# Kernel tuning notes

Measured on AMD Instinct MI355X. Metric: run time of the kernel, lower is better.

The kernel has to match this reference:

```python
import jax, jax.numpy as jnp
import numpy as np

B, C, MX, MY, MZ = 4, 64, 48, 48, 48
A, E = 64, 128  # n_atoms, mol_embed_size
V = MX * MY * MZ


def setup_inputs() -> dict:
    key = jax.random.key(0)
    ks = jax.random.split(key, 12)
    inp = {
        "x": jax.random.normal(ks[0], (B, C, MX, MY, MZ), dtype=jnp.float32),
        "mol_embed": jax.random.normal(ks[1], (B, A, E), dtype=jnp.float32),
        "pos": jax.random.uniform(ks[2], (B, A, 3), dtype=jnp.float32),
        "origin": jnp.zeros((B, 3), dtype=jnp.float32),
        "lattice": jax.random.uniform(ks[3], (B, 3, 3), dtype=jnp.float32) + 0.5,
        "batch_nodes": jax.random.randint(ks[4], (B,), 32, A + 1, dtype=jnp.int32),
        "v_w": jax.random.normal(ks[5], (C, E), dtype=jnp.float32) / np.sqrt(E),
        "v_b": jax.random.normal(ks[6], (C,), dtype=jnp.float32) * 0.01,
        "out_w": jax.random.normal(ks[7], (C, 2 * C), dtype=jnp.float32) / np.sqrt(2 * C),
        "out_b": jax.random.normal(ks[8], (C,), dtype=jnp.float32) * 0.01,
        "conv_w": jax.random.normal(ks[9], (C, C, 3, 3, 3), dtype=jnp.float32) / np.sqrt(C * 27),
        "conv_b": jax.random.normal(ks[10], (C,), dtype=jnp.float32) * 0.01,
    }
    return inp


def _grid_points(o, ldiag):
    # torch.linspace(o, o+l, n) inclusive endpoints -> t = arange(n)/(n-1)
    axes = [o[i] + ldiag[i] * (jnp.arange(n, dtype=jnp.float32) / (n - 1))
            for i, n in enumerate((MX, MY, MZ))]
    gx, gy, gz = jnp.meshgrid(*axes, indexing="ij")
    return jnp.stack([gx, gy, gz], axis=-1).reshape(-1, 3)  # [V,3]


def _forward(x, mol_embed, pos, origin, lattice, batch_nodes,
             v_w, v_b, out_w, out_b, conv_w, conv_b):
    b = x.shape[0]
    ldiag = jnp.diagonal(lattice, axis1=-2, axis2=-1)           # [b,3]
    grid = jax.vmap(_grid_points)(origin, ldiag)                # [b,V,3]
    # pairwise distances via |g|^2 + |p|^2 - 2 g.p (avoids [b,V,A,3])
    g2 = jnp.sum(grid * grid, axis=-1)                          # [b,V]
    p2 = jnp.sum(pos * pos, axis=-1)                            # [b,A]
    gp = jnp.einsum("bvd,bad->bva", grid, pos)                  # [b,V,A]
    d2 = g2[:, :, None] + p2[:, None, :] - 2.0 * gp
    dist = jnp.sqrt(jnp.maximum(d2, 1e-12))
    # ragged mask: atoms >= batch_nodes[i] get -inf score
    valid = jnp.arange(A)[None, None, :] < batch_nodes[:, None, None]
    weight = jnp.where(valid, -dist, -jnp.inf)
    att = jax.nn.softmax(weight, axis=-1)                       # [b,V,A]
    v = mol_embed @ v_w.T + v_b                                 # [b,A,C]
    v = jnp.einsum("bva,bac->bvc", att, v)                      # [b,V,C]
    xv = x.reshape(b, C, V).transpose(0, 2, 1)                  # [b,V,C]
    h = jnp.concatenate([xv, v], axis=-1)                       # [b,V,2C]
    h = jax.nn.relu(h @ out_w.T + out_b)                        # [b,V,C]
    h = h.transpose(0, 2, 1).reshape(b, C, MX, MY, MZ)
    hp = jnp.pad(h, ((0, 0), (0, 0), (1, 1), (1, 1), (1, 1)), mode="wrap")
    conv = jax.lax.conv_general_dilated(
        hp, conv_w, window_strides=(1, 1, 1), padding="VALID",
        dimension_numbers=("NCDHW", "OIDHW", "NCDHW"))
    conv = conv + conv_b[None, :, None, None, None]
    return jax.nn.relu(conv) + x


def reference(x, mol_embed, pos, origin, lattice, batch_nodes,
              v_w, v_b, out_w, out_b, conv_w, conv_b):
    return _forward(x, mol_embed, pos, origin, lattice, batch_nodes,
                    v_w, v_b, out_w, out_b, conv_w, conv_b)
```

## Files before the change

kernel.cpp:

```cpp
#include <hip/hip_runtime.h>

#define NB 4
#define NC 64
#define NV (48*48*48)
#define NA 64
#define NE 128

typedef __attribute__((ext_vector_type(8))) short short8;
typedef __attribute__((ext_vector_type(4))) float f32x4;

static __device__ __forceinline__ ushort f2bf(float f) {
  unsigned u = __float_as_uint(f);
  unsigned r = (u + 0x7FFF + ((u >> 16) & 1)) >> 16;
  return (ushort)r;
}
static __device__ __forceinline__ unsigned pk2bf(float lo, float hi) {
  return (unsigned)f2bf(lo) | ((unsigned)f2bf(hi) << 16);
}

__global__ __launch_bounds__(256) void k_prep(
    const float* __restrict__ me, const float* __restrict__ vw,
    const float* __restrict__ vb, const float* __restrict__ ow,
    ushort* __restrict__ BcT) {
  __shared__ float A[64 * 132];
  __shared__ float W[64 * 132];
  __shared__ float VM[64 * 68];
  int b = blockIdx.x, t = threadIdx.x;
  for (int i = t; i < 8192; i += 256) {
    A[(i >> 7) * 132 + (i & 127)] = me[b * 8192 + i];
    W[(i >> 7) * 132 + (i & 127)] = vw[i];
  }
  __syncthreads();
  for (int idx = t; idx < 4096; idx += 256) {
    int a = idx >> 6, c = idx & 63;
    float acc = vb[c];
#pragma unroll 8
    for (int e = 0; e < 128; e += 4) {
      float4 x4 = *(const float4*)&A[a * 132 + e];
      float4 w4 = *(const float4*)&W[c * 132 + e];
      acc += x4.x * w4.x + x4.y * w4.y + x4.z * w4.z + x4.w * w4.w;
    }
    VM[a * 68 + c] = acc;
  }
  __syncthreads();
  for (int i = t; i < 8192; i += 256)
    W[(i >> 7) * 132 + (i & 127)] = ow[i];
  __syncthreads();
  for (int idx = t; idx < 4096; idx += 256) {
    int o = idx >> 6, a = idx & 63;
    float acc = 0.f;
#pragma unroll 8
    for (int c = 0; c < 64; c += 4) {
      float4 v4 = *(const float4*)&VM[a * 68 + c];
      float4 w4 = *(const float4*)&W[o * 132 + 64 + c];
      acc += v4.x * w4.x + v4.y * w4.y + v4.z * w4.z + v4.w * w4.w;
    }
    BcT[b * 8192 + o * 128 + a] = f2bf(acc);
  }
  for (int idx = t; idx < 4096; idx += 256) {
    int o = idx >> 6, ci = idx & 63;
    BcT[b * 8192 + o * 128 + 64 + ci] = f2bf(W[o * 132 + ci]);
  }
}

__global__ void k_wt(const float* __restrict__ cw, ushort* __restrict__ wbf) {
  int idx = blockIdx.x * 256 + threadIdx.x;
  if (idx >= 27 * 64 * 64) return;
  int off = idx >> 12, r = idx & 4095;
  int kcw = r >> 11, r2 = r & 2047, nt = r2 >> 9, r3 = r2 & 511;
  int ln = r3 >> 3, e = r3 & 7;
  int co = nt * 16 + (ln & 15), ci = kcw * 32 + (ln >> 4) * 8 + e;
  wbf[idx] = f2bf(cw[(co * 64 + ci) * 27 + off]);
}

__global__ __launch_bounds__(256) void k_att2(
    const float* __restrict__ x, const float* __restrict__ pos,
    const float* __restrict__ origin, const float* __restrict__ lattice,
    const int* __restrict__ bnodes, const float* __restrict__ ob,
    const ushort* __restrict__ BcT, ushort* __restrict__ hbf) {
  __shared__ __align__(16) char Ac[32768];
  __shared__ float ps[192];
  __shared__ float sinv[128];
  int t = threadIdx.x;
  int lane = t & 63, wave = t >> 6;
  int b = blockIdx.y;
  int v0 = blockIdx.x * 128;
  int lm = lane & 15, lg = lane >> 4;

  short8 Bf[4][4];
  {
    const ushort* bp = BcT + b * 8192 + lm * 128 + lg * 8;
#pragma unroll
    for (int kb = 0; kb < 4; ++kb)
#pragma unroll
      for (int nt = 0; nt < 4; ++nt)
        Bf[kb][nt] = *(const short8*)(bp + nt * 2048 + kb * 32);
  }
  if (t < 192) ps[t] = pos[b * 192 + t];
  __syncthreads();

  {
    int v_loc = wave * 32 + (lane & 31);
    int half = lane >> 5;
    int v = v0 + v_loc;
    int ix = v / 2304;
    int rem = v - ix * 2304;
    int iy = rem / 48;
    int iz = rem - iy * 48;
    float gx = origin[b * 3 + 0] + lattice[b * 9 + 0] * (ix * (1.0f / 47.0f));
    float gy = origin[b * 3 + 1] + lattice[b * 9 + 4] * (iy * (1.0f / 47.0f));
    float gz = origin[b * 3 + 2] + lattice[b * 9 + 8] * (iz * (1.0f / 47.0f));
    int na = bnodes[b];
    int vswz = v_loc & 7;
    char* rowp = Ac + v_loc * 256;
    float s = 0.f;
#pragma unroll
    for (int i = 0; i < 32; i += 2) {
      float e2[2];
#pragma unroll
      for (int j = 0; j < 2; ++j) {
        int a = half * 32 + i + j;
        float dx = gx - ps[a * 3 + 0];
        float dy = gy - ps[a * 3 + 1];
        float dz = gz - ps[a * 3 + 2];
        float d = sqrtf(fmaxf(dx * dx + dy * dy + dz * dz, 1e-12f));
        float e = (a < na) ? __expf(-d) : 0.f;
        e2[j] = e;
        s += e;
      }
      int byteoff = (half * 32 + i) * 2;
      int slot = byteoff >> 4;
      *(unsigned*)(rowp + (((slot ^ vswz) << 4) | (byteoff & 15))) = pk2bf(e2[0], e2[1]);
    }
    s += __shfl_xor(s, 32);
    if (half == 0) sinv[v_loc] = 1.0f / s;
  }

  {
    int cp = t >> 3;
    int vq = t & 7;
    const float* xa = x + ((size_t)(b * 64 + 2 * cp)) * NV + v0 + vq * 16;
    const float* xb2 = xa + NV;
    int slot = 8 + (cp >> 2);
    int off = (cp & 3) * 4;
#pragma unroll
    for (int it = 0; it < 4; ++it) {
      float4 fa = *(const float4*)(xa + it * 4);
      float4 fb = *(const float4*)(xb2 + it * 4);
      int rbase = vq * 16 + it * 4;
#pragma unroll
      for (int j = 0; j < 4; ++j) {
        int row = rbase + j;
        float va = ((const float*)&fa)[j];
        float vb2 = ((const float*)&fb)[j];
        *(unsigned*)(Ac + row * 256 + (((slot ^ (row & 7)) << 4) | off)) = pk2bf(va, vb2);
      }
    }
  }
  __syncthreads();

  f32x4 acc[2][4];
#pragma unroll
  for (int mt = 0; mt < 2; ++mt)
#pragma unroll
    for (int nt = 0; nt < 4; ++nt) acc[mt][nt] = (f32x4){0.f, 0.f, 0.f, 0.f};

  auto do_k = [&](int kb) {
    short8 Af[2];
#pragma unroll
    for (int mt = 0; mt < 2; ++mt) {
      int row = wave * 32 + mt * 16 + lm;
      Af[mt] = *(const short8*)(Ac + row * 256 + ((((kb << 2) + lg) ^ (row & 7)) << 4));
    }
#pragma unroll
    for (int mt = 0; mt < 2; ++mt)
#pragma unroll
      for (int nt = 0; nt < 4; ++nt)
        acc[mt][nt] = __builtin_amdgcn_mfma_f32_16x16x32_bf16(Af[mt], Bf[kb][nt], acc[mt][nt], 0, 0, 0);
  };
  do_k(0);
  do_k(1);
#pragma unroll
  for (int mt = 0; mt < 2; ++mt) {
    float4 s4 = *(const float4*)&sinv[wave * 32 + mt * 16 + lg * 4];
#pragma unroll
    for (int nt = 0; nt < 4; ++nt) {
      acc[mt][nt][0] *= s4.x;
      acc[mt][nt][1] *= s4.y;
      acc[mt][nt][2] *= s4.z;
      acc[mt][nt][3] *= s4.w;
    }
  }
  do_k(2);
  do_k(3);

  __syncthreads();
  float bo[4];
#pragma unroll
  for (int nt = 0; nt < 4; ++nt) bo[nt] = ob[nt * 16 + lm];
#pragma unroll
  for (int mt = 0; mt < 2; ++mt)
#pragma unroll
    for (int nt = 0; nt < 4; ++nt) {
      int o = nt * 16 + lm;
      int slot = o >> 3;
      int off = (o & 7) * 2;
#pragma unroll
      for (int r = 0; r < 4; ++r) {
        int row = wave * 32 + mt * 16 + lg * 4 + r;
        float hv = fmaxf(acc[mt][nt][r] + bo[nt], 0.f);
        *(ushort*)(Ac + row * 128 + (((slot ^ (row & 7)) << 4) | off)) = f2bf(hv);
      }
    }
  __syncthreads();
  char* dst = (char*)hbf + ((size_t)(b * NV + v0)) * 128;
#pragma unroll
  for (int k = 0; k < 4; ++k) {
    int i = t + k * 256;
    int row = i >> 3, s = i & 7;
    *(uint4*)(dst + row * 128 + s * 16) =
        *(const uint4*)(Ac + row * 128 + ((s ^ (row & 7)) << 4));
  }
}

__global__ __launch_bounds__(256, 3) void k_conv(
    const ushort* __restrict__ hbf, const ushort* __restrict__ wbf,
    const float* __restrict__ cb, const float* __restrict__ x,
    float* __restrict__ out) {
  __shared__ __align__(16) char sm[36864];
  int t = threadIdx.x;
  int lane = t & 63, wave = t >> 6;
  int lm = lane & 15, lg = lane >> 4;
  int kc = wave >> 1;
  int mh = wave & 1;

  int bid = blockIdx.x;
  int sw = (bid & 7) * 576 + (bid >> 3);
  int b = sw / 1152, tid = sw - b * 1152;
  int xt = tid / 96, rem = tid - xt * 96, yt = rem >> 3, zt = rem & 7;
  int x0 = xt * 4, y0 = yt * 4, z0 = zt * 6;

  const char* hbase = (const char*)hbf + (size_t)b * NV * 128;
  const ushort* wl = wbf + kc * 2048 + lane * 8;

  short8 Ba[4], Bb[4], Bc[4];
#pragma unroll
  for (int nt = 0; nt < 4; ++nt) Ba[nt] = *(const short8*)(wl + nt * 512);
#pragma unroll
  for (int nt = 0; nt < 4; ++nt) Bb[nt] = *(const short8*)(wl + 4096 + nt * 512);

#pragma unroll
  for (int k = 0; k < 9; ++k) {
    int c = t + k * 256;
    int r = c >> 3, j = c & 7;
    int hx = r / 48, rr = r - hx * 48, hy = rr >> 3, hz = rr & 7;
    int gx = x0 + hx - 1; gx += (gx < 0) ? 48 : 0; gx -= (gx >= 48) ? 48 : 0;
    int gy = y0 + hy - 1; gy += (gy < 0) ? 48 : 0; gy -= (gy >= 48) ? 48 : 0;
    int gz = z0 + hz - 1; gz += (gz < 0) ? 48 : 0; gz -= (gz >= 48) ? 48 : 0;
    uint4 v = *(const uint4*)(hbase + (size_t)((gx * 2304 + gy * 48 + gz) * 128 + j * 16));
    *(uint4*)(sm + r * 128 + ((j ^ hz) << 4)) = v;
  }

  char* Abase[3][3];
#pragma unroll
  for (int mt = 0; mt < 3; ++mt) {
    int v = mt * 16 + lm;
    int xl = v / 24, rm2 = v - xl * 24, yl = rm2 / 6, zl = rm2 - yl * 6;
    int rowb = (mh * 2 + xl) * 48 + yl * 8 + zl;
#pragma unroll
    for (int dz = 0; dz < 3; ++dz)
      Abase[mt][dz] = sm + (rowb + dz) * 128 + ((((kc << 2) | lg) ^ (zl + dz)) << 4);
  }

  f32x4 acc[3][4];
#pragma unroll
  for (int i = 0; i < 3; ++i)
#pragma unroll
    for (int j = 0; j < 4; ++j) acc[i][j] = (f32x4){0.f, 0.f, 0.f, 0.f};

  __syncthreads();

  short8 Aa[3], Ab[3];
#pragma unroll
  for (int mt = 0; mt < 3; ++mt) Aa[mt] = *(const short8*)(Abase[mt][0]);

#define STEPC(o, Bcur, Bpre, Acur, Apre) { \
    if ((o) + 2 < 27) { \
      const ushort* p = wl + ((o) + 2) * 4096; \
      _Pragma("unroll") \
      for (int nt = 0; nt < 4; ++nt) Bpre[nt] = *(const short8*)(p + nt * 512); \
    } \
    if ((o) + 1 < 27) { \
      const int on = (o) + 1; \
      const int dxN = on / 9, dyzN = on - dxN * 9, dyN = dyzN / 3, dzN = dyzN - dyN * 3; \
      const int aimmN = (dxN * 48 + dyN * 8) * 128; \
      _Pragma("unroll") \
      for (int mt = 0; mt < 3; ++mt) Apre[mt] = *(const short8*)(Abase[mt][dzN] + aimmN); \
    } \
    __builtin_amdgcn_sched_barrier(0); \
    __builtin_amdgcn_s_setprio(1); \
    _Pragma("unroll") \
    for (int mt = 0; mt < 3; ++mt) \
      _Pragma("unroll") \
      for (int nt = 0; nt < 4; ++nt) \
        acc[mt][nt] = __builtin_amdgcn_mfma_f32_16x16x32_bf16(Acur[mt], Bcur[nt], acc[mt][nt], 0, 0, 0); \
    __builtin_amdgcn_s_setprio(0); \
    __builtin_amdgcn_sched_barrier(0); \
  }

  STEPC(0, Ba, Bc, Aa, Ab)  STEPC(1, Bb, Ba, Ab, Aa)  STEPC(2, Bc, Bb, Aa, Ab)
  STEPC(3, Ba, Bc, Ab, Aa)  STEPC(4, Bb, Ba, Aa, Ab)  STEPC(5, Bc, Bb, Ab, Aa)
  STEPC(6, Ba, Bc, Aa, Ab)  STEPC(7, Bb, Ba, Ab, Aa)  STEPC(8, Bc, Bb, Aa, Ab)
  STEPC(9, Ba, Bc, Ab, Aa)  STEPC(10, Bb, Ba, Aa, Ab) STEPC(11, Bc, Bb, Ab, Aa)
  STEPC(12, Ba, Bc, Aa, Ab) STEPC(13, Bb, Ba, Ab, Aa) STEPC(14, Bc, Bb, Aa, Ab)
  STEPC(15, Ba, Bc, Ab, Aa) STEPC(16, Bb, Ba, Aa, Ab) STEPC(17, Bc, Bb, Ab, Aa)
  STEPC(18, Ba, Bc, Aa, Ab) STEPC(19, Bb, Ba, Ab, Aa) STEPC(20, Bc, Bb, Aa, Ab)
  STEPC(21, Ba, Bc, Ab, Aa) STEPC(22, Bb, Ba, Aa, Ab) STEPC(23, Bc, Bb, Ab, Aa)
  STEPC(24, Ba, Bc, Aa, Ab) STEPC(25, Bb, Ba, Ab, Aa) STEPC(26, Bc, Bb, Aa, Ab)
#undef STEPC

  const float* xb = x + (size_t)b * NC * NV;
  float* obp = out + (size_t)b * NC * NV;
  float2 xr2[6][2];
  size_t gaddr[6][2];
#pragma unroll
  for (int k = 0; k < 6; ++k) {
    int c = t + k * 256;
    int co = c / 24, q = c - co * 24;
#pragma unroll
    for (int p = 0; p < 2; ++p) {
      int v = q * 4 + p * 2;
      int xl = v / 24, rm = v - xl * 24, yl = rm / 6, zl = rm - yl * 6;
      size_t g = (size_t)co * NV + (x0 + xl) * 2304 + (y0 + yl) * 48 + (z0 + zl);
      gaddr[k][p] = g;
      xr2[k][p] = *(const float2*)(xb + g);
    }
  }

  __syncthreads();
  float* red = (float*)sm;
  if (kc == 1) {
#pragma unroll
    for (int mt = 0; mt < 3; ++mt)
#pragma unroll
      for (int nt = 0; nt < 4; ++nt) {
        int co = nt * 16 + lm;
        int vox = mh * 48 + mt * 16 + lg * 4;
        *(float4*)&red[co * 104 + vox] = (float4){acc[mt][nt][0], acc[mt][nt][1],
                                                  acc[mt][nt][2], acc[mt][nt][3]};
      }
  }
  __syncthreads();
  if (kc == 0) {
    float bo[4];
#pragma unroll
    for (int nt = 0; nt < 4; ++nt) bo[nt] = cb[nt * 16 + lm];
#pragma unroll
    for (int mt = 0; mt < 3; ++mt)
#pragma unroll
      for (int nt = 0; nt < 4; ++nt) {
        int co = nt * 16 + lm;
        int vox = mh * 48 + mt * 16 + lg * 4;
        float4 p = *(const float4*)&red[co * 104 + vox];
        float4 r;
        r.x = fmaxf(acc[mt][nt][0] + p.x + bo[nt], 0.f);
        r.y = fmaxf(acc[mt][nt][1] + p.y + bo[nt], 0.f);
        r.z = fmaxf(acc[mt][nt][2] + p.z + bo[nt], 0.f);
        r.w = fmaxf(acc[mt][nt][3] + p.w + bo[nt], 0.f);
        *(float4*)&red[co * 104 + vox] = r;
      }
  }
  __syncthreads();
#pragma unroll
  for (int k = 0; k < 6; ++k) {
    int c = t + k * 256;
    int co = c / 24, q = c - co * 24;
#pragma unroll
    for (int p = 0; p < 2; ++p) {
      int v = q * 4 + p * 2;
      float2 rv = *(const float2*)&red[co * 104 + v];
      float2 o2;
      o2.x = rv.x + xr2[k][p].x;
      o2.y = rv.y + xr2[k][p].y;
      *(float2*)(obp + gaddr[k][p]) = o2;
    }
  }
}

extern "C" void kernel_launch(void* const* d_in, const int* in_sizes, int n_in,
                              void* d_out, int out_size, void* d_ws, size_t ws_size,
                              hipStream_t stream) {
  const float* x = (const float*)d_in[0];
  const float* me = (const float*)d_in[1];
  const float* pos = (const float*)d_in[2];
  const float* origin = (const float*)d_in[3];
  const float* lattice = (const float*)d_in[4];
  const int* bn = (const int*)d_in[5];
  const float* vw = (const float*)d_in[6];
  const float* vb = (const float*)d_in[7];
  const float* ow = (const float*)d_in[8];
  const float* ob = (const float*)d_in[9];
  const float* cw = (const float*)d_in[10];
  const float* cbias = (const float*)d_in[11];
  float* outp = (float*)d_out;

  ushort* BcT = (ushort*)d_ws;
  ushort* wbf = (ushort*)((char*)d_ws + 65536);
  ushort* hbf = (ushort*)((char*)d_ws + 65536 + 221184);

  k_prep<<<NB, 256, 0, stream>>>(me, vw, vb, ow, BcT);
  k_wt<<<(27 * 64 * 64 + 255) / 256, 256, 0, stream>>>(cw, wbf);
  k_att2<<<dim3(NV / 128, NB), 256, 0, stream>>>(x, pos, origin, lattice, bn, ob, BcT, hbf);
  k_conv<<<4608, 256, 0, stream>>>(hbf, wbf, cbias, x, outp);
}
```

Before: 214.5 us.

## Split prep kernel across more blocks and prefetch x loads before attention math

The single 4-block prep kernel is split into two kernels: one computing mol_embed@v_w^T over 64 blocks, and one folding the result into out_w over 32 blocks. This spreads a serial-ish prologue across more CUs. In the attention kernel, the x tile loads are issued into registers up front, with a sched barrier, so their latency overlaps the distance/exp computation. The cost is an extra launch, a scratch buffer aliased onto hbf, and higher register pressure.

```diff
diff --git a/kernel.cpp b/kernel.cpp
--- a/kernel.cpp
+++ b/kernel.cpp
@@ -18,48 +18,60 @@
   return (unsigned)f2bf(lo) | ((unsigned)f2bf(hi) << 16);
 }
 
-__global__ __launch_bounds__(256) void k_prep(
+__global__ __launch_bounds__(256) void k_vm(
     const float* __restrict__ me, const float* __restrict__ vw,
-    const float* __restrict__ vb, const float* __restrict__ ow,
+    const float* __restrict__ vb, float* __restrict__ vmat) {
+  int blk = blockIdx.x;
+  int b = blk >> 4, aq = blk & 15;
+  int t = threadIdx.x;
+  int a = aq * 4 + (t >> 6);
+  int c = t & 63;
+  const float* mp = me + (size_t)(b * 64 + a) * 128;
+  const float* wp = vw + (size_t)c * 128;
+  float acc = vb[c];
+#pragma unroll 8
+  for (int e = 0; e < 128; e += 4) {
+    float4 m4 = *(const float4*)(mp + e);
+    float4 w4 = *(const float4*)(wp + e);
+    acc += m4.x * w4.x + m4.y * w4.y + m4.z * w4.z + m4.w * w4.w;
+  }
+  vmat[b * 4096 + a * 64 + c] = acc;
+}
+
+__global__ __launch_bounds__(256) void k_bct(
+    const float* __restrict__ ow, const float* __restrict__ vmat,
     ushort* __restrict__ BcT) {
-  __shared__ float A[64 * 132];
-  __shared__ float W[64 * 132];
   __shared__ float VM[64 * 68];
-  int b = blockIdx.x, t = threadIdx.x;
-  for (int i = t; i < 8192; i += 256) {
-    A[(i >> 7) * 132 + (i & 127)] = me[b * 8192 + i];
-    W[(i >> 7) * 132 + (i & 127)] = vw[i];
-  }
-  __syncthreads();
-  for (int idx = t; idx < 4096; idx += 256) {
-    int a = idx >> 6, c = idx & 63;
-    float acc = vb[c];
-#pragma unroll 8
-    for (int e = 0; e < 128; e += 4) {
-      float4 x4 = *(const float4*)&A[a * 132 + e];
-      float4 w4 = *(const float4*)&W[c * 132 + e];
-      acc += x4.x * w4.x + x4.y * w4.y + x4.z * w4.z + x4.w * w4.w;
-    }
-    VM[a * 68 + c] = acc;
-  }
-  __syncthreads();
-  for (int i = t; i < 8192; i += 256)
-    W[(i >> 7) * 132 + (i & 127)] = ow[i];
-  __syncthreads();
-  for (int idx = t; idx < 4096; idx += 256) {
-    int o = idx >> 6, a = idx & 63;
+  __shared__ float WV[8 * 68];
+  int blk = blockIdx.x;
+  int b = blk >> 3, og = blk & 7;
+  int t = threadIdx.x;
+  for (int i = t; i < 4096; i += 256)
+    VM[(i >> 6) * 68 + (i & 63)] = vmat[b * 4096 + i];
+  for (int i = t; i < 512; i += 256)
+    WV[(i >> 6) * 68 + (i & 63)] = ow[(og * 8 + (i >> 6)) * 128 + 64 + (i & 63)];
+  __syncthreads();
+  int ol = t >> 5;
+  int a0 = (t & 31) * 2;
+  int o = og * 8 + ol;
+#pragma unroll
+  for (int p = 0; p < 2; ++p) {
+    int a = a0 + p;
     float acc = 0.f;
 #pragma unroll 8
     for (int c = 0; c < 64; c += 4) {
       float4 v4 = *(const float4*)&VM[a * 68 + c];
-      float4 w4 = *(const float4*)&W[o * 132 + 64 + c];
+      float4 w4 = *(const float4*)&WV[ol * 68 + c];
       acc += v4.x * w4.x + v4.y * w4.y + v4.z * w4.z + v4.w * w4.w;
     }
     BcT[b * 8192 + o * 128 + a] = f2bf(acc);
   }
-  for (int idx = t; idx < 4096; idx += 256) {
-    int o = idx >> 6, ci = idx & 63;
-    BcT[b * 8192 + o * 128 + 64 + ci] = f2bf(W[o * 132 + ci]);
+#pragma unroll
+  for (int p = 0; p < 2; ++p) {
+    int i = t * 2 + p;
+    int ol2 = i >> 6, ci = i & 63;
+    int o2 = og * 8 + ol2;
+    BcT[b * 8192 + o2 * 128 + 64 + ci] = f2bf(ow[o2 * 128 + ci]);
   }
 }
 
@@ -87,6 +99,19 @@
   int v0 = blockIdx.x * 128;
   int lm = lane & 15, lg = lane >> 4;
 
+  if (t < 192) ps[t] = pos[b * 192 + t];
+  __syncthreads();
+
+  int cp = t >> 3;
+  int vq = t & 7;
+  const float* xa = x + ((size_t)(b * 64 + 2 * cp)) * NV + v0 + vq * 16;
+  const float* xb2 = xa + NV;
+  float4 fa[4], fb[4];
+#pragma unroll
+  for (int it = 0; it < 4; ++it) {
+    fa[it] = *(const float4*)(xa + it * 4);
+    fb[it] = *(const float4*)(xb2 + it * 4);
+  }
   short8 Bf[4][4];
   {
     const ushort* bp = BcT + b * 8192 + lm * 128 + lg * 8;
@@ -96,8 +121,7 @@
       for (int nt = 0; nt < 4; ++nt)
         Bf[kb][nt] = *(const short8*)(bp + nt * 2048 + kb * 32);
   }
-  if (t < 192) ps[t] = pos[b * 192 + t];
-  __syncthreads();
+  __builtin_amdgcn_sched_barrier(0);
 
   {
     int v_loc = wave * 32 + (lane & 31);
@@ -137,22 +161,16 @@
   }
 
   {
-    int cp = t >> 3;
-    int vq = t & 7;
-    const float* xa = x + ((size_t)(b * 64 + 2 * cp)) * NV + v0 + vq * 16;
-    const float* xb2 = xa + NV;
     int slot = 8 + (cp >> 2);
     int off = (cp & 3) * 4;
 #pragma unroll
     for (int it = 0; it < 4; ++it) {
-      float4 fa = *(const float4*)(xa + it * 4);
-      float4 fb = *(const float4*)(xb2 + it * 4);
       int rbase = vq * 16 + it * 4;
 #pragma unroll
       for (int j = 0; j < 4; ++j) {
         int row = rbase + j;
-        float va = ((const float*)&fa)[j];
-        float vb2 = ((const float*)&fb)[j];
+        float va = ((const float*)&fa[it])[j];
+        float vb2 = ((const float*)&fb[it])[j];
         *(unsigned*)(Ac + row * 256 + (((slot ^ (row & 7)) << 4) | off)) = pk2bf(va, vb2);
       }
     }
@@ -407,8 +425,10 @@
   ushort* BcT = (ushort*)d_ws;
   ushort* wbf = (ushort*)((char*)d_ws + 65536);
   ushort* hbf = (ushort*)((char*)d_ws + 65536 + 221184);
-
-  k_prep<<<NB, 256, 0, stream>>>(me, vw, vb, ow, BcT);
+  float* vmat = (float*)hbf;
+
+  k_vm<<<64, 256, 0, stream>>>(me, vw, vb, vmat);
+  k_bct<<<32, 256, 0, stream>>>(ow, vmat, BcT);
   k_wt<<<(27 * 64 * 64 + 255) / 256, 256, 0, stream>>>(cw, wbf);
   k_att2<<<dim3(NV / 128, NB), 256, 0, stream>>>(x, pos, origin, lattice, bn, ob, BcT, hbf);
   k_conv<<<4608, 256, 0, stream>>>(hbf, wbf, cbias, x, outp);
```

Measured after the change: 210.0 us. 1.02x faster.
